# Kernel tuning notes

Measured on AMD Instinct MI355X. Metric: run time of the kernel, lower is better.

The kernel has to match this reference:

```python
import jax, jax.numpy as jnp
import numpy as np

CAPACITY = 60.0
CONS_RATE = 0.2
T_LIMIT = 11.0
VELOCITY = 60.0
NUM_AFS = 3
BS, SEQ, H = 256, 256, 128
NEG = -1e9


def setup_inputs() -> dict:
    key = jax.random.key(0)
    ks = jax.random.split(key, 12)
    coords = jax.random.uniform(ks[0], (BS, SEQ, 2))
    static = jnp.transpose(coords, (0, 2, 1))  # [bs, 2, seq]
    diff = coords[:, :, None, :] - coords[:, None, :, :]
    distances = jnp.sqrt(jnp.sum(diff * diff, -1) + 1e-12)  # [bs, seq, seq]
    demands = jax.random.uniform(ks[1], (BS, SEQ), minval=0.1, maxval=1.0)
    demands = demands.at[:, :NUM_AFS + 1].set(0.0)  # depot + AFS have no demand
    dynamic = jnp.stack([jnp.full((BS, SEQ), CAPACITY),
                         jnp.full((BS, SEQ), T_LIMIT),
                         demands], axis=1)  # [bs, 3, seq]
    p = lambda k, shape: 0.1 * jax.random.normal(k, shape)
    return dict(
        static=static, dynamic=dynamic, distances=distances,
        W_s=p(ks[2], (H, 2)), b_s=jnp.zeros(H),
        W_d=p(ks[3], (H, 3)), b_d=jnp.zeros(H),
        W_i=p(ks[4], (4 * H, H)), W_h=p(ks[5], (4 * H, H)),
        b_i=jnp.zeros(4 * H), b_h=jnp.zeros(4 * H),
        W_att=p(ks[6], (H, 3 * H)), v_att=p(ks[7], (H,)),
        W_c=p(ks[8], (H, 2 * H)), b_c=jnp.zeros(H),
        decode_steps=128)


def reference(static, dynamic, distances, W_s, b_s, W_d, b_d, W_i, W_h, b_i, b_h,
              W_att, v_att, W_c, b_c, decode_steps):
    bs, _, seq = static.shape
    h = W_s.shape[0]
    arange_b = jnp.arange(bs)
    node_ids = jnp.arange(seq)

    # Encoder = Conv1d(kernel=1): [bs,c,seq] -> [bs,h,seq]
    stat_emb = jnp.einsum('oc,bcs->bos', W_s, static) + b_s[None, :, None]

    # dis_by_afs: cheapest via-AFS distance from each node to depot
    dba = jnp.stack([distances[:, i, 0:1] + distances[:, i, :]
                     for i in range(1, NUM_AFS + 1)], 1)  # [bs, num_afs, seq]
    dis_by_afs = jnp.min(dba, axis=1).at[:, 0].set(0.0)    # [bs, seq]

    fuel0 = dynamic[:, 0, 0]
    time0 = dynamic[:, 1, 0]
    dem0 = dynamic[:, 2, :]
    ones_seq = jnp.ones((1, seq), static.dtype)

    def enc_dyn(fuel, time, dem):
        dyn = jnp.stack([fuel[:, None] * ones_seq, time[:, None] * ones_seq, dem], 1)
        return jnp.einsum('oc,bcs->bos', W_d, dyn) + b_d[None, :, None]

    def step(carry, key):
        fuel, time, dem, hst, cst, old_idx, dec_in, mask = carry
        dyn_emb = enc_dyn(fuel, time, dem)
        # one LSTM step (PyTorch gate order i,f,g,o)
        gates = dec_in @ W_i.T + hst @ W_h.T + b_i + b_h
        ig, fg, gg, og = jnp.split(gates, 4, axis=-1)
        cst = jax.nn.sigmoid(fg) * cst + jax.nn.sigmoid(ig) * jnp.tanh(gg)
        h_lstm = jax.nn.sigmoid(og) * jnp.tanh(cst)
        # pointer attention over nodes
        feat = jnp.concatenate(
            [stat_emb, dyn_emb, jnp.broadcast_to(h_lstm[:, :, None], (bs, h, seq))], axis=1)
        e = jnp.einsum('k,bks->bs', v_att,
                       jnp.tanh(jnp.einsum('kc,bcs->bks', W_att, feat)))
        logits = jnp.where(mask, e, NEG)
        idx = jax.random.categorical(key, logits)               # sample next node
        logp = jax.nn.log_softmax(logits)[arange_b, idx]
        probs = jax.nn.softmax(logits)
        context = jnp.einsum('bs,bhs->bh', probs, stat_emb)
        h_new = jnp.tanh(jnp.concatenate([context, h_lstm], -1) @ W_c.T + b_c)
        # update_fn: fuel/time/demand dynamics + feasibility mask
        dis = distances[arange_b, old_idx, idx]
        fuel = fuel - CONS_RATE * dis
        time = time - dis / VELOCITY
        at_dep = idx == 0
        at_af = (idx >= 1) & (idx <= NUM_AFS)
        fuel = jnp.where(at_dep | at_af, CAPACITY, fuel)
        time = jnp.where(at_dep, T_LIMIT, time)
        dem = dem.at[arange_b, idx].set(jnp.where(idx > NUM_AFS, 0.0, dem[arange_b, idx]))
        d_next = distances[arange_b, idx, :]  # [bs, seq]
        fuel_ok = fuel[:, None] >= CONS_RATE * (d_next + dis_by_afs)
        time_ok = time[:, None] >= (d_next + distances[:, :, 0]) / VELOCITY
        cust_mask = (dem > 0) & fuel_ok & time_ok
        depot_af_mask = node_ids[None, :] != idx[:, None]
        mask = jnp.where(node_ids[None, :] <= NUM_AFS, depot_af_mask, cust_mask)
        mask = mask.at[:, 0].set(True)  # depot always reachable -> no all-masked rows
        dec_in = stat_emb[arange_b, :, idx]
        return (fuel, time, dem, h_new, cst, idx, dec_in, mask), (probs, idx, logp)

    init = (fuel0, time0, dem0,
            jnp.zeros((bs, h)), jnp.zeros((bs, h)),
            jnp.zeros(bs, jnp.int32), stat_emb[:, :, 0],
            jnp.ones((bs, seq), bool))
    keys = jax.random.split(jax.random.key(1), decode_steps)
    _, (probs, tours, logps) = jax.lax.scan(step, init, keys)
    # outputs [bs, T, seq], tours [bs, T], tour_logp [bs, T]
    return jnp.transpose(probs, (1, 0, 2)), tours.T, logps.T
```

## Files before the change

kernel.cpp:

```cpp
#include <hip/hip_runtime.h>
#include <cmath>

#define BSZ 256
#define SEQN 256
#define HD 128
#define NEGV -1000000000.0f
#define TINYF 1.17549435e-38f
#define LOG2E 1.4426950408889634f
#define LN2F 0.6931471805599453f
#define K2L 2.885390081777927f

typedef float v2f __attribute__((ext_vector_type(2)));

static __device__ __forceinline__ v2f mk2(float a, float b) {
  v2f r; r.x = a; r.y = b; return r;
}
static __device__ __forceinline__ v2f fma2(v2f a, v2f b, v2f c) {
  return __builtin_elementwise_fma(a, b, c);
}

#define DPPF(x, c) __int_as_float(__builtin_amdgcn_update_dpp(0, __float_as_int(x), (c), 0xF, 0xF, true))
#define DPPI(x, c) __builtin_amdgcn_update_dpp(0, (x), (c), 0xF, 0xF, true)
#define SWZF(x, p) __int_as_float(__builtin_amdgcn_ds_swizzle(__float_as_int(x), (p)))

static __device__ __forceinline__ void tf2x32(unsigned k0, unsigned k1,
                                              unsigned x0, unsigned x1,
                                              unsigned &o0, unsigned &o1) {
  unsigned ks2 = k0 ^ k1 ^ 0x1BD11BDAu;
#define TFR(r) { x0 += x1; x1 = (x1 << (r)) | (x1 >> (32 - (r))); x1 ^= x0; }
  x0 += k0; x1 += k1;
  TFR(13) TFR(15) TFR(26) TFR(6)
  x0 += k1; x1 += ks2 + 1u;
  TFR(17) TFR(29) TFR(16) TFR(24)
  x0 += ks2; x1 += k0 + 2u;
  TFR(13) TFR(15) TFR(26) TFR(6)
  x0 += k0; x1 += k1 + 3u;
  TFR(17) TFR(29) TFR(16) TFR(24)
  x0 += k1; x1 += ks2 + 4u;
  TFR(13) TFR(15) TFR(26) TFR(6)
  x0 += ks2; x1 += k0 + 5u;
#undef TFR
  o0 = x0; o1 = x1;
}

static __device__ __forceinline__ float fast_tanh(float x) {
  float y = __fmul_rn(x, K2L);
  float ay = __int_as_float(__float_as_int(y) | 0x80000000u);
  float q = __builtin_amdgcn_exp2f(ay);
  float r = __fmul_rn(__fsub_rn(1.0f, q),
                      __builtin_amdgcn_rcpf(__fadd_rn(1.0f, q)));
  unsigned sgn = (unsigned)__float_as_int(x) & 0x80000000u;
  return __int_as_float(__float_as_int(r) | sgn);
}

static __device__ __forceinline__ float fast_sig(float x) {
  float q = __builtin_amdgcn_exp2f(__fmul_rn(x, -LOG2E));
  return __builtin_amdgcn_rcpf(__fadd_rn(1.0f, q));
}

static __device__ __forceinline__ float fast_ln(float x) {
  return __fmul_rn(__builtin_amdgcn_logf(x), LN2F);
}

__global__ __launch_bounds__(512, 2) void evrp_kernel(
    const float* __restrict__ statc, const float* __restrict__ dyn,
    const float* __restrict__ dist,  const float* __restrict__ W_s,
    const float* __restrict__ b_s,   const float* __restrict__ W_d,
    const float* __restrict__ b_d,   const float* __restrict__ W_i,
    const float* __restrict__ W_h,   const float* __restrict__ b_i,
    const float* __restrict__ b_h,   const float* __restrict__ W_att,
    const float* __restrict__ v_att, const float* __restrict__ W_c,
    const float* __restrict__ b_c,   const int* __restrict__ steps_p,
    float* __restrict__ out) {
  const int b = blockIdx.x;
  const int tid = threadIdx.x;
  const int T = steps_p[0];
  const int lane = tid & 63;
  const int wv = tid >> 6;
  const int s = tid >> 1, hf = tid & 1;
  const int cq = tid >> 2, g = tid & 3;

  extern __shared__ __align__(16) float4 Pdyn[];

  __shared__ __align__(16) float  B0a[HD], B1a[HD], A2a[HD];
  __shared__ __align__(16) float  Ct[HD], Vt[HD];
  __shared__ __align__(16) float  hstm[HD], hlm[HD], wc2v[HD];
  __shared__ __align__(16) float  A0a[HD], A1a[HD], D0a[HD];
  __shared__ __align__(16) float  C0a[HD], C1a[HD], C2a[HD], bca[HD];
  __shared__ __align__(16) float2 xy2[SEQN];
  __shared__ __align__(16) float  drowX[SEQN];
  __shared__ __align__(16) unsigned kAs[256], kBs[256];
  __shared__ __align__(16) float ws0[HD], ws1[HD], bsv[HD];
  __shared__ __align__(16) float wd0[HD], wd1[HD], wd2[HD], bdv[HD];
  __shared__ __align__(16) float2 wredA[8];
  __shared__ __align__(16) float4 wredB[8];

  const float* distb = dist + (size_t)b * SEQN * SEQN;

  if (tid < HD) {
    ws0[tid] = W_s[2 * tid]; ws1[tid] = W_s[2 * tid + 1]; bsv[tid] = b_s[tid];
    wd0[tid] = W_d[3 * tid]; wd1[tid] = W_d[3 * tid + 1]; wd2[tid] = W_d[3 * tid + 2];
    bdv[tid] = b_d[tid]; bca[tid] = b_c[tid];
    hstm[tid] = 0.0f;
  }
  float xreg = statc[b * 2 * SEQN + s];
  float yreg = statc[b * 2 * SEQN + SEQN + s];
  float demreg = dyn[b * 3 * SEQN + 2 * SEQN + s];
  float d2dR = distb[(size_t)s * SEQN];
  float dbaR;
  {
    float d10 = distb[1 * SEQN + 0], d20 = distb[2 * SEQN + 0], d30 = distb[3 * SEQN + 0];
    float d1s = distb[1 * SEQN + s], d2s = distb[2 * SEQN + s], d3s = distb[3 * SEQN + s];
    float m = fminf(fminf(__fadd_rn(d10, d1s), __fadd_rn(d20, d2s)), __fadd_rn(d30, d3s));
    dbaR = (s == 0) ? 0.0f : m;
  }
  float dnextR = distb[s];
  if (hf == 0) xy2[s] = make_float2(xreg, yreg);
  float fuelR = dyn[b * 3 * SEQN + 0];
  float timeR = dyn[b * 3 * SEQN + SEQN + 0];
  float cstR = 0.0f;
  int niR = 0;
  for (int tt = tid; tt < 256; tt += 512) {
    unsigned a0, a1; tf2x32(0u, 1u, 0u, (unsigned)tt, a0, a1);
    kAs[tt] = a0; kBs[tt] = a1;
  }
  __syncthreads();

  if (tid < HD) {
    int k = tid;
    const float* row = W_att + (size_t)k * 384;
    float B0 = 0, B1 = 0, B2 = 0, A0 = 0, A1 = 0, A2 = 0, A3 = 0;
    for (int c = 0; c < HD; ++c) {
      float w1 = row[c], w2 = row[128 + c];
      B0 = fmaf(w1, ws0[c], B0); B1 = fmaf(w1, ws1[c], B1); B2 = fmaf(w1, bsv[c], B2);
      A0 = fmaf(w2, wd0[c], A0); A1 = fmaf(w2, wd1[c], A1);
      A2 = fmaf(w2, wd2[c], A2); A3 = fmaf(w2, bdv[c], A3);
    }
    B0a[k] = B0; B1a[k] = B1; A2a[k] = A2; Vt[k] = v_att[k];
    A0a[k] = A0; A1a[k] = A1; D0a[k] = __fadd_rn(B2, A3);
  } else if (tid < 2 * HD) {
    int o = tid - HD;
    const float* row = W_c + (size_t)o * 256;
    float C0 = 0, C1 = 0, C2 = 0;
    for (int c = 0; c < HD; ++c) {
      float w = row[c];
      C0 = fmaf(w, ws0[c], C0); C1 = fmaf(w, ws1[c], C1); C2 = fmaf(w, bsv[c], C2);
    }
    C0a[o] = C0; C1a[o] = C1; C2a[o] = C2;
  }
  float gp0 = 0, gp1 = 0, gp2 = 0, gpw;
  {
    int j = g * HD + cq;
    const float* row = W_i + (size_t)j * HD;
    for (int c = 0; c < HD; ++c) {
      float w = row[c];
      gp0 = fmaf(w, ws0[c], gp0); gp1 = fmaf(w, ws1[c], gp1); gp2 = fmaf(w, bsv[c], gp2);
    }
    gpw = __fadd_rn(b_i[j], b_h[j]);
  }
  v2f whreg2[HD / 2];
  {
    int j = g * HD + cq;
#pragma unroll
    for (int c2 = 0; c2 < HD / 2; ++c2)
      whreg2[c2] = *(const v2f*)(&W_h[(size_t)j * HD + 2 * c2]);
  }
  v2f wah2[16], wc22[16];
#pragma unroll
  for (int i = 0; i < 16; ++i) {
    wah2[i] = *(const v2f*)(&W_att[(size_t)cq * 384 + 256 + g * 32 + 2 * i]);
    wc22[i] = *(const v2f*)(&W_c[(size_t)cq * 256 + HD + g * 32 + 2 * i]);
  }
#pragma unroll
  for (int c = 0; c < HD / 2; c += 2)
    asm volatile("" : "+v"(whreg2[c]), "+v"(whreg2[c + 1]));
#pragma unroll
  for (int i = 0; i < 16; i += 2) {
    asm volatile("" : "+v"(wah2[i]), "+v"(wah2[i + 1]));
    asm volatile("" : "+v"(wc22[i]), "+v"(wc22[i + 1]));
  }
  __syncthreads();

  for (int idx = tid; idx < SEQN * HD; idx += 512) {
    int ss = idx >> 7, k = idx & 127;
    float2 pxy = xy2[ss];
    float dm = dyn[b * 3 * SEQN + 2 * SEQN + ss];
    float pv = fmaf(B0a[k], pxy.x, fmaf(B1a[k], pxy.y, __fmul_rn(A2a[k], dm)));
    ((float*)Pdyn)[(((k >> 2) & 15) << 11) + ((ss * 2 + (k >> 6)) << 2) + (k & 3)] =
        __builtin_amdgcn_exp2f(__fmul_rn(pv, K2L));
  }
  float Vsum = 0.0f;
#pragma unroll
  for (int i = 0; i < 32; ++i) {
    float4 v4 = ((const float4*)Vt)[i];
    Vsum = __fadd_rn(Vsum, __fadd_rn(__fadd_rn(v4.x, v4.y), __fadd_rn(v4.z, v4.w)));
  }
  __syncthreads();

  float decxR = xy2[0].x, decyR = xy2[0].y;

  float* out_probs = out;
  float* out_tours = out + (size_t)BSZ * T * SEQN;
  float* out_logps = out_tours + (size_t)BSZ * T;

  const float4* Pp = Pdyn + (s * 2 + hf);
  const float* CtH = Ct + hf * 64;
  const float* VtH = Vt + hf * 64;

  float prevPr = 0.0f, prevLp = 0.0f;
  int prevNi = 0;

  for (int t = 0; t < T; ++t) {
    if (t > 0) {
      if (hf == 0) out_probs[((size_t)b * T + (t - 1)) * SEQN + s] = prevPr;
      if (s == prevNi && hf == 0) {
        out_tours[(size_t)b * T + (t - 1)] = (float)prevNi;
        out_logps[(size_t)b * T + (t - 1)] = prevLp;
      }
      dnextR = distb[(size_t)niR * SEQN + s];
    }
    {
      v2f mA0 = mk2(0.f, 0.f), mB0 = mk2(0.f, 0.f);
      v2f mA1 = mk2(0.f, 0.f), mB1 = mk2(0.f, 0.f);
      const float4* h4 = (const float4*)hstm;
#pragma unroll
      for (int c8 = 0; c8 < HD / 8; ++c8) {
        float4 h0 = h4[2 * c8], h1 = h4[2 * c8 + 1];
        mA0 = fma2(whreg2[4 * c8 + 0], mk2(h0.x, h0.y), mA0);
        mB0 = fma2(whreg2[4 * c8 + 1], mk2(h0.z, h0.w), mB0);
        mA1 = fma2(whreg2[4 * c8 + 2], mk2(h1.x, h1.y), mA1);
        mB1 = fma2(whreg2[4 * c8 + 3], mk2(h1.z, h1.w), mB1);
      }
      float md = fmaf(gp0, decxR, fmaf(gp1, decyR, gp2));
      float mh = __fadd_rn(
          __fadd_rn(__fadd_rn(mA0.x, mA0.y), __fadd_rn(mB0.x, mB0.y)),
          __fadd_rn(__fadd_rn(mA1.x, mA1.y), __fadd_rn(mB1.x, mB1.y)));
      float V = __fadd_rn(__fadd_rn(md, mh), gpw);
      float sg = fast_sig(V), th = fast_tanh(V);
      float q = (g == 2) ? th : sg;
      float u1 = DPPF(q, 0xB1);
      float u2 = DPPF(q, 0x4E);
      float u3 = DPPF(q, 0x1B);
      float qi = (g == 0) ? q  : (g == 1) ? u1 : (g == 2) ? u2 : u3;
      float qf = (g == 0) ? u1 : (g == 1) ? q  : (g == 2) ? u3 : u2;
      float qg = (g == 0) ? u2 : (g == 1) ? u3 : (g == 2) ? q  : u1;
      float qo = (g == 0) ? u3 : (g == 1) ? u2 : (g == 2) ? u1 : q;
      float cn = __fadd_rn(__fmul_rn(qf, cstR), __fmul_rn(qi, qg));
      cstR = cn;
      float hv = __fmul_rn(qo, fast_tanh(cn));
      if (g == 0) hlm[(cq & 96) | ((cq & 31) ^ ((cq >> 5) << 3))] = hv;
    }
    __syncthreads();
    {
      v2f pwA = mk2(0.f, 0.f), pwB = mk2(0.f, 0.f);
      v2f pcA = mk2(0.f, 0.f), pcB = mk2(0.f, 0.f);
      const float4* hl4 = (const float4*)hlm;
#pragma unroll
      for (int l4 = 0; l4 < 8; ++l4) {
        float4 hh = hl4[(g << 3) + (l4 ^ (g << 1))];
        v2f hA = mk2(hh.x, hh.y), hB = mk2(hh.z, hh.w);
        pwA = fma2(wah2[2 * l4],     hA, pwA);
        pwB = fma2(wah2[2 * l4 + 1], hB, pwB);
        pcA = fma2(wc22[2 * l4],     hA, pcA);
        pcB = fma2(wc22[2 * l4 + 1], hB, pcB);
      }
      float pw = __fadd_rn(__fadd_rn(pwA.x, pwA.y), __fadd_rn(pwB.x, pwB.y));
      float pc = __fadd_rn(__fadd_rn(pcA.x, pcA.y), __fadd_rn(pcB.x, pcB.y));
      pw = __fadd_rn(pw, DPPF(pw, 0xB1));
      pc = __fadd_rn(pc, DPPF(pc, 0xB1));
      pw = __fadd_rn(pw, DPPF(pw, 0x4E));
      pc = __fadd_rn(pc, DPPF(pc, 0x4E));
      if (g == 0) {
        wc2v[cq] = pc;
        float Ck = fmaf(A0a[cq], fuelR, fmaf(A1a[cq], timeR, __fadd_rn(D0a[cq], pw)));
        Ct[cq] = __builtin_amdgcn_exp2f(__fmul_rn(Ck, K2L));
      }
    }
    __syncthreads();
    float pe, lg;
    if (hf == 0) drowX[s] = dnextR;
    bool mk;
    if (t == 0) mk = true;
    else {
      bool fok = fuelR >= __fmul_rn(0.2f, __fadd_rn(dnextR, dbaR));
      bool tok = timeR >= __fdiv_rn(__fadd_rn(dnextR, d2dR), 60.0f);
      bool cust = (demreg > 0.0f) && fok && tok;
      mk = (s <= 3) ? (s != niR) : cust;
      if (s == 0) mk = true;
    }
    {
      unsigned rb;
      { unsigned o0, o1; tf2x32(kAs[t], kBs[t], 0u, (unsigned)(b * SEQN + s), o0, o1); rb = o0 ^ o1; }
      float f = __uint_as_float((rb >> 9) | 0x3f800000u) - 1.0f;
      float u = fmaxf(TINYF, __fadd_rn(f, TINYF));
      float gmb = -fast_ln(-fast_ln(u));
      const v2f one2 = mk2(1.0f, 1.0f);
      v2f a0 = mk2(0.f, 0.f), a1 = mk2(0.f, 0.f);
      v2f a2 = mk2(0.f, 0.f), a3 = mk2(0.f, 0.f);
#pragma unroll
      for (int i = 0; i < 8; ++i) {
        float4 pv0 = Pp[(2 * i) << 9];
        float4 ct0 = *(const float4*)(CtH + 8 * i);
        float4 vv0 = *(const float4*)(VtH + 8 * i);
        v2f sA = mk2(pv0.x, pv0.y) * mk2(ct0.x, ct0.y) + one2;
        v2f sB = mk2(pv0.z, pv0.w) * mk2(ct0.z, ct0.w) + one2;
        v2f rA, rB;
        rA.x = __builtin_amdgcn_rcpf(sA.x); rA.y = __builtin_amdgcn_rcpf(sA.y);
        rB.x = __builtin_amdgcn_rcpf(sB.x); rB.y = __builtin_amdgcn_rcpf(sB.y);
        a0 = fma2(mk2(vv0.x, vv0.y), rA, a0);
        a1 = fma2(mk2(vv0.z, vv0.w), rB, a1);
        float4 pv1 = Pp[(2 * i + 1) << 9];
        float4 ct1 = *(const float4*)(CtH + 8 * i + 4);
        float4 vv1 = *(const float4*)(VtH + 8 * i + 4);
        v2f sC = mk2(pv1.x, pv1.y) * mk2(ct1.x, ct1.y) + one2;
        v2f sD = mk2(pv1.z, pv1.w) * mk2(ct1.z, ct1.w) + one2;
        v2f rC, rD;
        rC.x = __builtin_amdgcn_rcpf(sC.x); rC.y = __builtin_amdgcn_rcpf(sC.y);
        rD.x = __builtin_amdgcn_rcpf(sD.x); rD.y = __builtin_amdgcn_rcpf(sD.y);
        a2 = fma2(mk2(vv1.x, vv1.y), rC, a2);
        a3 = fma2(mk2(vv1.z, vv1.w), rD, a3);
      }
      v2f t01 = a0 + a1, t23 = a2 + a3;
      v2f tt = t01 + t23;
      float part = __fadd_rn(tt.x, tt.y);
      float tot = __fadd_rn(part, DPPF(part, 0xB1));
      float e = fmaf(-2.0f, tot, Vsum);
      lg = mk ? e : NEGV;
      pe = __builtin_amdgcn_exp2f(__fmul_rn(lg, LOG2E));
      float sc = __fadd_rn(gmb, lg);
      float av = sc; int ai = s;
      float S = pe, px = __fmul_rn(pe, xreg), py = __fmul_rn(pe, yreg);
      {
        float ov = DPPF(av, 0x4E); int oi = DPPI(ai, 0x4E);
        if (ov > av || (ov == av && oi < ai)) { av = ov; ai = oi; }
        S  = __fadd_rn(S,  DPPF(S,  0x4E));
        px = __fadd_rn(px, DPPF(px, 0x4E));
        py = __fadd_rn(py, DPPF(py, 0x4E));
      }
      {
        float ov = DPPF(av, 0x124); int oi = DPPI(ai, 0x124);
        if (ov > av || (ov == av && oi < ai)) { av = ov; ai = oi; }
        S  = __fadd_rn(S,  DPPF(S,  0x124));
        px = __fadd_rn(px, DPPF(px, 0x124));
        py = __fadd_rn(py, DPPF(py, 0x124));
      }
      {
        float ov = DPPF(av, 0x128); int oi = DPPI(ai, 0x128);
        if (ov > av || (ov == av && oi < ai)) { av = ov; ai = oi; }
        S  = __fadd_rn(S,  DPPF(S,  0x128));
        px = __fadd_rn(px, DPPF(px, 0x128));
        py = __fadd_rn(py, DPPF(py, 0x128));
      }
      {
        float ov = SWZF(av, 0x401F); int oi = __builtin_amdgcn_ds_swizzle(ai, 0x401F);
        if (ov > av || (ov == av && oi < ai)) { av = ov; ai = oi; }
        S  = __fadd_rn(S,  SWZF(S,  0x401F));
        px = __fadd_rn(px, SWZF(px, 0x401F));
        py = __fadd_rn(py, SWZF(py, 0x401F));
      }
      {
        float ov = __shfl_xor(av, 32, 64); int oi = __shfl_xor(ai, 32, 64);
        if (ov > av || (ov == av && oi < ai)) { av = ov; ai = oi; }
        S  = __fadd_rn(S,  __shfl_xor(S,  32, 64));
        px = __fadd_rn(px, __shfl_xor(px, 32, 64));
        py = __fadd_rn(py, __shfl_xor(py, 32, 64));
      }
      if (lane == 0) {
        wredA[wv] = make_float2(av, (float)ai);
        wredB[wv] = make_float4(S, px, py, 0.0f);
      }
    }
    __syncthreads();
    {
      float2 a0c = wredA[0];
      float bv = a0c.x; int bi = (int)a0c.y;
#pragma unroll
      for (int w = 1; w < 8; ++w) {
        float2 aw = wredA[w];
        if (aw.x > bv) { bv = aw.x; bi = (int)aw.y; }
      }
      int ni = bi;
      float4 b0 = wredB[0];
      float S = b0.x, px = b0.y, py = b0.z;
#pragma unroll
      for (int w = 1; w < 8; ++w) {
        float4 bw = wredB[w];
        S = __fadd_rn(S, bw.x); px = __fadd_rn(px, bw.y); py = __fadd_rn(py, bw.z);
      }
      float dis = drowX[ni];
      float fl = __fsub_rn(fuelR, __fmul_rn(0.2f, dis));
      float tm = __fsub_rn(timeR, __fdiv_rn(dis, 60.0f));
      if (ni <= 3) fl = 60.0f;
      if (ni == 0) tm = 11.0f;
      fuelR = fl; timeR = tm;
      if (s == ni && ni > 3) demreg = 0.0f;
      float2 dxy = xy2[ni];
      decxR = dxy.x; decyR = dxy.y;
      prevPr = __fdiv_rn(pe, S);
      prevLp = __fsub_rn(lg, fast_ln(S));
      prevNi = ni;
      if (tid < HD) {
        float cx = __fdiv_rn(px, S), cy = __fdiv_rn(py, S);
        float ctxd = fmaf(C0a[tid], cx, fmaf(C1a[tid], cy, C2a[tid]));
        float val = __fadd_rn(__fadd_rn(ctxd, wc2v[tid]), bca[tid]);
        hstm[tid] = fast_tanh(val);
      }
      niR = ni;
    }
    __syncthreads();
  }
  if (hf == 0) out_probs[((size_t)b * T + (T - 1)) * SEQN + s] = prevPr;
  if (s == prevNi && hf == 0) {
    out_tours[(size_t)b * T + (T - 1)] = (float)prevNi;
    out_logps[(size_t)b * T + (T - 1)] = prevLp;
  }
}

extern "C" void kernel_launch(void* const* d_in, const int* in_sizes, int n_in,
                              void* d_out, int out_size, void* d_ws, size_t ws_size,
                              hipStream_t stream) {
  (void)in_sizes; (void)n_in; (void)out_size; (void)d_ws; (void)ws_size;
  (void)hipFuncSetAttribute((const void*)evrp_kernel,
                            hipFuncAttributeMaxDynamicSharedMemorySize,
                            SEQN * HD * 4);
  evrp_kernel<<<dim3(BSZ), dim3(512), SEQN * HD * 4, stream>>>(
      (const float*)d_in[0],  (const float*)d_in[1],  (const float*)d_in[2],
      (const float*)d_in[3],  (const float*)d_in[4],  (const float*)d_in[5],
      (const float*)d_in[6],  (const float*)d_in[7],  (const float*)d_in[8],
      (const float*)d_in[9],  (const float*)d_in[10], (const float*)d_in[11],
      (const float*)d_in[12], (const float*)d_in[13], (const float*)d_in[14],
      (const int*)d_in[15],   (float*)d_out);
}
```

Measured before the change: 747.2 us.

## Precompute Gumbel noise in a separate parallel kernel and read it per step

Adds a gumbel_fill kernel that generates the threefry Gumbel noise for every (batch, step, node) into the workspace before the main decode kernel. The serial decode loop then loads one precomputed float per step instead of running threefry and two logs on its critical path. It also partially unrolls two inner loops and removes register-pinning asm on some weights, likely to lower register pressure. The cost is an extra launch plus writing and reading BSZ*T*SEQN floats of global memory, and if the workspace is too small it falls back to computing the noise inline.

Measured after the change: 1.480 ms. +98.0%, slower.

```diff
diff --git a/kernel.cpp b/kernel.cpp
--- a/kernel.cpp
+++ b/kernel.cpp
@@ -62,6 +62,25 @@
   return __fmul_rn(__builtin_amdgcn_logf(x), LN2F);
 }
 
+static __device__ __forceinline__ float gumbel_of(int b, int t, int s) {
+  unsigned k0, k1, o0, o1;
+  tf2x32(0u, 1u, 0u, (unsigned)t, k0, k1);
+  tf2x32(k0, k1, 0u, (unsigned)(b * SEQN + s), o0, o1);
+  unsigned rb = o0 ^ o1;
+  float f = __uint_as_float((rb >> 9) | 0x3f800000u) - 1.0f;
+  float u = fmaxf(TINYF, __fadd_rn(f, TINYF));
+  return -fast_ln(-fast_ln(u));
+}
+
+__global__ __launch_bounds__(512) void gumbel_fill(float* __restrict__ gws, int T) {
+  int idx = blockIdx.x * 512 + threadIdx.x;
+  if (idx >= BSZ * T * SEQN) return;
+  int s = idx & (SEQN - 1);
+  int bt = idx >> 8;
+  int t = bt % T, b = bt / T;
+  gws[idx] = gumbel_of(b, t, s);
+}
+
 __global__ __launch_bounds__(512, 2) void evrp_kernel(
     const float* __restrict__ statc, const float* __restrict__ dyn,
     const float* __restrict__ dist,  const float* __restrict__ W_s,
@@ -71,7 +90,7 @@
     const float* __restrict__ b_h,   const float* __restrict__ W_att,
     const float* __restrict__ v_att, const float* __restrict__ W_c,
     const float* __restrict__ b_c,   const int* __restrict__ steps_p,
-    float* __restrict__ out) {
+    const float* __restrict__ gws,   float* __restrict__ out) {
   const int b = blockIdx.x;
   const int tid = threadIdx.x;
   const int T = steps_p[0];
@@ -174,11 +193,6 @@
 #pragma unroll
   for (int c = 0; c < HD / 2; c += 2)
     asm volatile("" : "+v"(whreg2[c]), "+v"(whreg2[c + 1]));
-#pragma unroll
-  for (int i = 0; i < 16; i += 2) {
-    asm volatile("" : "+v"(wah2[i]), "+v"(wah2[i + 1]));
-    asm volatile("" : "+v"(wc22[i]), "+v"(wc22[i + 1]));
-  }
   __syncthreads();
 
   for (int idx = tid; idx < SEQN * HD; idx += 512) {
@@ -211,6 +225,9 @@
   int prevNi = 0;
 
   for (int t = 0; t < T; ++t) {
+    float gmbR;
+    if (gws) gmbR = gws[((size_t)b * T + t) * SEQN + s];
+    else     gmbR = gumbel_of(b, t, s);
     if (t > 0) {
       if (hf == 0) out_probs[((size_t)b * T + (t - 1)) * SEQN + s] = prevPr;
       if (s == prevNi && hf == 0) {
@@ -223,7 +240,7 @@
       v2f mA0 = mk2(0.f, 0.f), mB0 = mk2(0.f, 0.f);
       v2f mA1 = mk2(0.f, 0.f), mB1 = mk2(0.f, 0.f);
       const float4* h4 = (const float4*)hstm;
-#pragma unroll
+#pragma unroll 4
       for (int c8 = 0; c8 < HD / 8; ++c8) {
         float4 h0 = h4[2 * c8], h1 = h4[2 * c8 + 1];
         mA0 = fma2(whreg2[4 * c8 + 0], mk2(h0.x, h0.y), mA0);
@@ -289,15 +306,10 @@
       if (s == 0) mk = true;
     }
     {
-      unsigned rb;
-      { unsigned o0, o1; tf2x32(kAs[t], kBs[t], 0u, (unsigned)(b * SEQN + s), o0, o1); rb = o0 ^ o1; }
-      float f = __uint_as_float((rb >> 9) | 0x3f800000u) - 1.0f;
-      float u = fmaxf(TINYF, __fadd_rn(f, TINYF));
-      float gmb = -fast_ln(-fast_ln(u));
       const v2f one2 = mk2(1.0f, 1.0f);
       v2f a0 = mk2(0.f, 0.f), a1 = mk2(0.f, 0.f);
       v2f a2 = mk2(0.f, 0.f), a3 = mk2(0.f, 0.f);
-#pragma unroll
+#pragma unroll 2
       for (int i = 0; i < 8; ++i) {
         float4 pv0 = Pp[(2 * i) << 9];
         float4 ct0 = *(const float4*)(CtH + 8 * i);
@@ -327,7 +339,7 @@
       float e = fmaf(-2.0f, tot, Vsum);
       lg = mk ? e : NEGV;
       pe = __builtin_amdgcn_exp2f(__fmul_rn(lg, LOG2E));
-      float sc = __fadd_rn(gmb, lg);
+      float sc = __fadd_rn(gmbR, lg);
       float av = sc; int ai = s;
       float S = pe, px = __fmul_rn(pe, xreg), py = __fmul_rn(pe, yreg);
       {
@@ -419,7 +431,15 @@
 extern "C" void kernel_launch(void* const* d_in, const int* in_sizes, int n_in,
                               void* d_out, int out_size, void* d_ws, size_t ws_size,
                               hipStream_t stream) {
-  (void)in_sizes; (void)n_in; (void)out_size; (void)d_ws; (void)ws_size;
+  (void)in_sizes; (void)n_in;
+  int T = out_size / (BSZ * (SEQN + 2));
+  size_t need = (size_t)BSZ * T * SEQN * sizeof(float);
+  float* gws = nullptr;
+  if (d_ws && ws_size >= need && T > 0) {
+    gws = (float*)d_ws;
+    int total = BSZ * T * SEQN;
+    gumbel_fill<<<dim3((total + 511) / 512), dim3(512), 0, stream>>>(gws, T);
+  }
   (void)hipFuncSetAttribute((const void*)evrp_kernel,
                             hipFuncAttributeMaxDynamicSharedMemorySize,
                             SEQN * HD * 4);
@@ -429,5 +449,5 @@
       (const float*)d_in[6],  (const float*)d_in[7],  (const float*)d_in[8],
       (const float*)d_in[9],  (const float*)d_in[10], (const float*)d_in[11],
       (const float*)d_in[12], (const float*)d_in[13], (const float*)d_in[14],
-      (const int*)d_in[15],   (float*)d_out);
-}
+      (const int*)d_in[15],   gws, (float*)d_out);
+}
```
